# Kernel optimization log

Measured on AMD Instinct MI355X. Metric: run time of the kernel, lower is better.

Reference implementation:

```python
import jax, jax.numpy as jnp
import numpy as np

B, T, D, H = 2, 2048, 1024, 16
HD = D // H  # head dim = 64

def setup_inputs() -> dict:
    key = jax.random.key(0)
    k1, k2, k3 = jax.random.split(key, 3)
    x = jax.random.normal(k1, (B, T, D), dtype=jnp.float32)
    W_qkv = jax.random.normal(k2, (D, 3 * D), dtype=jnp.float32) * 0.02
    b_qkv = jax.random.normal(k3, (3 * D,), dtype=jnp.float32) * 0.02
    return {"x": x, "W_qkv": W_qkv, "b_qkv": b_qkv}

def reference(x, W_qkv, b_qkv):
    Bc, Tc, C = x.shape
    qkv = x @ W_qkv + b_qkv                     # [B,T,3D]
    q, k, v = jnp.split(qkv, 3, axis=-1)        # each [B,T,D]
    def to_heads(t):
        return t.reshape(Bc, Tc, H, HD).transpose(0, 2, 1, 3)  # [B,H,T,hd]
    q, k, v = to_heads(q), to_heads(k), to_heads(v)
    scale = 1.0 / jnp.sqrt(jnp.asarray(HD, dtype=x.dtype))
    att = jnp.einsum('bhqd,bhkd->bhqk', q, k) * scale  # [B,H,T,T]
    att = jax.nn.softmax(att, axis=-1)
    y = jnp.einsum('bhqk,bhkd->bhqd', att, v)          # [B,H,T,hd]
    return y.transpose(0, 2, 1, 3).reshape(Bc, Tc, C)
```

## Files before the change

### kernel.cpp

```cpp
#include <hip/hip_runtime.h>
#include <cstdint>

typedef unsigned short u16;
typedef __bf16 bf16x8 __attribute__((ext_vector_type(8)));
typedef float f32x4 __attribute__((ext_vector_type(4)));
typedef u16 u16x4 __attribute__((ext_vector_type(4)));
typedef u16 u16x8 __attribute__((ext_vector_type(8)));

static __device__ __forceinline__ u16 f2bf(float f) {
  return __builtin_bit_cast(u16, (__bf16)f);
}
static __device__ __forceinline__ float fexp2(float x) {
  float r;
  asm("v_exp_f32 %0, %1" : "=v"(r) : "v"(x));
  return r;
}

#define GLOAD16(gsrc, ldst) \
  __builtin_amdgcn_global_load_lds((const __attribute__((address_space(1))) void*)(gsrc), \
                                   (__attribute__((address_space(3))) void*)(ldst), 16, 0, 0)


__global__ __launch_bounds__(256) void k_prep(const float* __restrict__ x,
                                              const float* __restrict__ W,
                                              u16* __restrict__ xbf,
                                              u16* __restrict__ Wt) {
  __shared__ __align__(16) u16 tile[64 * 72];
  int t = threadIdx.x;
  if (blockIdx.x < 2048) {
    int idx = blockIdx.x * 256 + t;
    const float4* xv = (const float4*)x;
    float4 a = xv[(size_t)idx * 2];
    float4 b = xv[(size_t)idx * 2 + 1];
    u16x8 o;
    o[0]=f2bf(a.x); o[1]=f2bf(a.y); o[2]=f2bf(a.z); o[3]=f2bf(a.w);
    o[4]=f2bf(b.x); o[5]=f2bf(b.y); o[6]=f2bf(b.z); o[7]=f2bf(b.w);
    *(u16x8*)(xbf + (size_t)idx * 8) = o;
    return;
  }
  int bid = blockIdx.x - 2048;
  int bk = bid & 15, bn = bid >> 4;
  int k0 = bk * 64, n0 = bn * 64;
  #pragma unroll
  for (int r = 0; r < 4; r++) {
    int id = r * 256 + t;
    int kl = id >> 4;
    int c  = (id & 15) * 4;
    float4 v = *(const float4*)(W + (size_t)(k0 + kl) * 3072 + n0 + c);
    u16x4 o; o[0]=f2bf(v.x); o[1]=f2bf(v.y); o[2]=f2bf(v.z); o[3]=f2bf(v.w);
    *(u16x4*)(tile + kl * 72 + c) = o;
  }
  __syncthreads();
  #pragma unroll
  for (int r = 0; r < 2; r++) {
    int id = r * 256 + t;
    int nl = id >> 3;
    int w  = id & 7;
    u16x8 o;
    #pragma unroll
    for (int i = 0; i < 8; i++) o[i] = tile[(w * 8 + i) * 72 + nl];
    *(u16x8*)(Wt + (size_t)(n0 + nl) * 1024 + k0 + w * 8) = o;
  }
}

__global__ __launch_bounds__(256) void k_gemm_qkv(const u16* __restrict__ xbf,
                                                  const u16* __restrict__ wt,
                                                  const float* __restrict__ bias,
                                                  u16* __restrict__ qkv,
                                                  u16* __restrict__ vT) {
  __shared__ __align__(16) u16 As[128 * 32];
  __shared__ __align__(16) u16 Bs[128 * 32];
  int bid = blockIdx.x;
  int nt = bid % 24, mt = bid / 24;
  int m0 = mt * 128, n0 = nt * 128;
  int t = threadIdx.x;
  int lane = t & 63, wave = t >> 6;
  int wm = wave >> 1, wn = wave & 1;
  int g = lane >> 4, li = lane & 15;

  f32x4 acc[4][4];
  #pragma unroll
  for (int i = 0; i < 4; i++)
    #pragma unroll
    for (int j = 0; j < 4; j++) acc[i][j] = (f32x4){0.f, 0.f, 0.f, 0.f};

  for (int kt = 0; kt < 32; ++kt) {
    __syncthreads();
    #pragma unroll
    for (int r = 0; r < 2; r++) {
      int p = r * 256 + t;
      int row = p >> 2, w = p & 3;
      int ug = w ^ ((row >> 1) & 3);
      GLOAD16(xbf + (size_t)(m0 + row) * 1024 + kt * 32 + ug * 8, (char*)As + p * 16);
      GLOAD16(wt  + (size_t)(n0 + row) * 1024 + kt * 32 + ug * 8, (char*)Bs + p * 16);
    }
    asm volatile("s_waitcnt vmcnt(0)" ::: "memory");
    __syncthreads();

    bf16x8 af[4], bfr[4];
    #pragma unroll
    for (int mi = 0; mi < 4; mi++) {
      int row = wm * 64 + mi * 16 + li;
      int u = g ^ ((row >> 1) & 3);
      af[mi] = *(const bf16x8*)((const char*)As + row * 64 + u * 16);
    }
    #pragma unroll
    for (int ni = 0; ni < 4; ni++) {
      int row = wn * 64 + ni * 16 + li;
      int u = g ^ ((row >> 1) & 3);
      bfr[ni] = *(const bf16x8*)((const char*)Bs + row * 64 + u * 16);
    }
    #pragma unroll
    for (int mi = 0; mi < 4; mi++)
      #pragma unroll
      for (int ni = 0; ni < 4; ni++)
        acc[mi][ni] = __builtin_amdgcn_mfma_f32_16x16x32_bf16(af[mi], bfr[ni], acc[mi][ni], 0, 0, 0);
  }

  int b = m0 >> 11;
  int tbase = m0 & 2047;
  #pragma unroll
  for (int ni = 0; ni < 4; ni++) {
    int col = n0 + wn * 64 + ni * 16 + li;
    float bv = bias[col];
    float sc = (col < 1024) ? 0.18033688011112042f : 1.0f;
    #pragma unroll
    for (int mi = 0; mi < 4; mi++) {
      int trow = tbase + wm * 64 + mi * 16 + g * 4;
      if (col < 2048) {
        #pragma unroll
        for (int j = 0; j < 4; j++) {
          float v = (acc[mi][ni][j] + bv) * sc;
          qkv[(size_t)(b * 2048 + trow + j) * 3072 + col] = f2bf(v);
        }
      } else {
        u16x4 o;
        #pragma unroll
        for (int j = 0; j < 4; j++) o[j] = f2bf(acc[mi][ni][j] + bv);
        *(u16x4*)(vT + ((size_t)(b * 1024 + (col - 2048))) * 2048 + trow) = o;
      }
    }
  }
}

__global__ __launch_bounds__(256, 2) void k_attn(const u16* __restrict__ qkv,
                                                 const u16* __restrict__ vT,
                                                 float* __restrict__ out) {
  __shared__ __align__(16) u16 smem[32768];
  int bid = blockIdx.x;
  int qt = bid & 15, bh = bid >> 4;
  int b = bh >> 4, h = bh & 15;
  int qbase = qt * 128;
  int t = threadIdx.x, lane = t & 63, wave = t >> 6;
  int g = lane >> 4, li = lane & 15;

  size_t qrowa = (size_t)(b * 2048 + qbase + wave * 32 + li) * 3072 + h * 64;
  bf16x8 qa0 = *(const bf16x8*)(qkv + qrowa + g * 8);
  bf16x8 qa1 = *(const bf16x8*)(qkv + qrowa + 32 + g * 8);
  bf16x8 qb0 = *(const bf16x8*)(qkv + qrowa + 16 * 3072 + g * 8);
  bf16x8 qb1 = *(const bf16x8*)(qkv + qrowa + 16 * 3072 + 32 + g * 8);

  u16x8 ob; 
  #pragma unroll
  for (int i = 0; i < 8; i++) ob[i] = 0x3F80;
  bf16x8 ones = __builtin_bit_cast(bf16x8, ob);

  f32x4 o[2][4];
  #pragma unroll
  for (int f = 0; f < 2; f++)
    #pragma unroll
    for (int i = 0; i < 4; i++) o[f][i] = (f32x4){0.f, 0.f, 0.f, 0.f};
  f32x4 la = (f32x4){0.f, 0.f, 0.f, 0.f}, lb = la;

  const u16* kbase_g = qkv + (size_t)(b * 2048) * 3072 + 1024 + h * 64;
  const u16* vbase_g = vT + (size_t)(bh * 64) * 2048;

  int kRow[4], kUg[4], vRow[4], vUg[4];
  #pragma unroll
  for (int i = 0; i < 4; i++) {
    int p = t + i * 256;
    int kr = p >> 3;
    kRow[i] = (kr & 96) | ((kr & 16) >> 2) | (((kr >> 2) & 3) << 3) | (kr & 3);
    kUg[i] = (p & 7) ^ (kr & 7);
    int vd = p >> 4;
    vRow[i] = vd;
    vUg[i] = (p & 15) ^ (vd & 7);
  }

  auto stage = [&](int key0, int buf) {
    char* kd = (char*)smem + buf * 16384;
    char* vd_ = (char*)smem + 32768 + buf * 16384;
    #pragma unroll
    for (int i = 0; i < 4; i++) {
      int p = t + i * 256;
      GLOAD16(kbase_g + (size_t)(key0 + kRow[i]) * 3072 + kUg[i] * 8, kd + p * 16);
      GLOAD16(vbase_g + (size_t)vRow[i] * 2048 + key0 + vUg[i] * 8, vd_ + p * 16);
    }
  };

  stage(0, 0);
  asm volatile("s_waitcnt vmcnt(0)" ::: "memory");
  __syncthreads();

  #pragma unroll 2
  for (int ph = 0; ph < 16; ++ph) {
    int buf = ph & 1;
    const char* kb = (const char*)smem + buf * 16384;
    const char* vb = (const char*)smem + 32768 + buf * 16384;

    if (ph < 15) stage((ph + 1) * 128, buf ^ 1);

    #pragma unroll
    for (int h2 = 0; h2 < 2; ++h2) {
      const char* kbh = kb + h2 * 8192;
      f32x4 sa[4], sb[4];
      int u0 = g ^ (li & 7);
      __builtin_amdgcn_s_setprio(1);
      #pragma unroll
      for (int st = 0; st < 4; ++st) {
        bf16x8 kf0 = *(const bf16x8*)(kbh + (st * 16 + li) * 128 + u0 * 16);
        bf16x8 kf1 = *(const bf16x8*)(kbh + (st * 16 + li) * 128 + (u0 ^ 4) * 16);
        f32x4 z = (f32x4){0.f, 0.f, 0.f, 0.f};
        sa[st] = __builtin_amdgcn_mfma_f32_16x16x32_bf16(kf0, qa0, z, 0, 0, 0);
        sa[st] = __builtin_amdgcn_mfma_f32_16x16x32_bf16(kf1, qa1, sa[st], 0, 0, 0);
        sb[st] = __builtin_amdgcn_mfma_f32_16x16x32_bf16(kf0, qb0, z, 0, 0, 0);
        sb[st] = __builtin_amdgcn_mfma_f32_16x16x32_bf16(kf1, qb1, sb[st], 0, 0, 0);
      }
      __builtin_amdgcn_s_setprio(0);

      float pa[16], pbf[16];
      #pragma unroll
      for (int i = 0; i < 16; i++) pa[i] = fexp2(sa[i >> 2][i & 3]);
      #pragma unroll
      for (int i = 0; i < 16; i++) pbf[i] = fexp2(sb[i >> 2][i & 3]);

      bf16x8 pba[2], pbb[2];
      #pragma unroll
      for (int c = 0; c < 2; c++)
        #pragma unroll
        for (int e = 0; e < 8; e++) {
          pba[c][e] = (__bf16)pa[c * 8 + e];
          pbb[c][e] = (__bf16)pbf[c * 8 + e];
        }

      __builtin_amdgcn_s_setprio(1);
      la = __builtin_amdgcn_mfma_f32_16x16x32_bf16(ones, pba[0], la, 0, 0, 0);
      la = __builtin_amdgcn_mfma_f32_16x16x32_bf16(ones, pba[1], la, 0, 0, 0);
      lb = __builtin_amdgcn_mfma_f32_16x16x32_bf16(ones, pbb[0], lb, 0, 0, 0);
      lb = __builtin_amdgcn_mfma_f32_16x16x32_bf16(ones, pbb[1], lb, 0, 0, 0);
      #pragma unroll
      for (int c = 0; c < 2; c++) {
        int ucb = h2 * 8 + c * 4 + g;
        #pragma unroll
        for (int dt = 0; dt < 4; dt++) {
          int d = dt * 16 + li;
          bf16x8 vf = *(const bf16x8*)(vb + d * 256 + ((ucb ^ (li & 7)) << 4));
          o[0][dt] = __builtin_amdgcn_mfma_f32_16x16x32_bf16(vf, pba[c], o[0][dt], 0, 0, 0);
          o[1][dt] = __builtin_amdgcn_mfma_f32_16x16x32_bf16(vf, pbb[c], o[1][dt], 0, 0, 0);
        }
      }
      __builtin_amdgcn_s_setprio(0);
    }

    __syncthreads();
  }

  float inva = 1.0f / la[0], invb = 1.0f / lb[0];
  #pragma unroll
  for (int f = 0; f < 2; f++) {
    float inv = f ? invb : inva;
    int ql = wave * 32 + f * 16 + li;
    #pragma unroll
    for (int dt = 0; dt < 4; dt++) {
      int u = dt * 4 + g;
      int up = u ^ (ql & 7);
      f32x4 v = o[f][dt] * inv;
      *(f32x4*)((char*)smem + ql * 256 + up * 16) = v;
    }
  }
  __syncthreads();
  int ql = t >> 1, seg = t & 1;
  size_t obase = (size_t)(b * 2048 + qbase + ql) * 1024 + h * 64;
  #pragma unroll
  for (int i = 0; i < 8; i++) {
    int u = seg * 8 + i;
    int up = u ^ (ql & 7);
    f32x4 v = *(const f32x4*)((const char*)smem + ql * 256 + up * 16);
    *(f32x4*)(out + obase + u * 4) = v;
  }
}

extern "C" void kernel_launch(void* const* d_in, const int* in_sizes, int n_in,
                              void* d_out, int out_size, void* d_ws, size_t ws_size,
                              hipStream_t stream) {
  const float* x    = (const float*)d_in[0];
  const float* W    = (const float*)d_in[1];
  const float* bias = (const float*)d_in[2];
  float* out = (float*)d_out;
  char* ws = (char*)d_ws;
  u16* xbf = (u16*)(ws + 0);
  u16* wt  = (u16*)(ws + 8388608);
  u16* qkv = (u16*)(ws + 14680064);
  u16* vt  = (u16*)(ws + 39845888);

  k_prep<<<2816, 256, 0, stream>>>(x, W, xbf, wt);
  k_gemm_qkv<<<768, 256, 0, stream>>>(xbf, wt, bias, qkv, vt);
  k_attn<<<512, 256, 0, stream>>>(qkv, vt, out);
}
```

Baseline: 93.60 us.

## Retile QKV GEMM to 256x192 with double-buffered LDS and grid swizzle

```diff
diff --git a/kernel.cpp b/kernel.cpp
--- a/kernel.cpp
+++ b/kernel.cpp
@@ -63,70 +63,86 @@
   }
 }
 
-__global__ __launch_bounds__(256) void k_gemm_qkv(const u16* __restrict__ xbf,
-                                                  const u16* __restrict__ wt,
-                                                  const float* __restrict__ bias,
-                                                  u16* __restrict__ qkv,
-                                                  u16* __restrict__ vT) {
-  __shared__ __align__(16) u16 As[128 * 32];
-  __shared__ __align__(16) u16 Bs[128 * 32];
-  int bid = blockIdx.x;
-  int nt = bid % 24, mt = bid / 24;
-  int m0 = mt * 128, n0 = nt * 128;
+__global__ __launch_bounds__(512, 2) void k_gemm_qkv(const u16* __restrict__ xbf,
+                                                     const u16* __restrict__ wt,
+                                                     const float* __restrict__ bias,
+                                                     u16* __restrict__ qkv,
+                                                     u16* __restrict__ vT) {
+  __shared__ __align__(16) u16 As[2 * 256 * 32];
+  __shared__ __align__(16) u16 Bs[2 * 192 * 32];
+  int wg = blockIdx.x;
+  int swz = (wg & 7) * 32 + (wg >> 3);
+  int mt = swz >> 4, nt = swz & 15;
+  int m0 = mt * 256, n0 = nt * 192;
   int t = threadIdx.x;
-  int lane = t & 63, wave = t >> 6;
-  int wm = wave >> 1, wn = wave & 1;
+  int lane = t & 63, wid = t >> 6;
+  int wm = wid >> 2, wn = wid & 3;
   int g = lane >> 4, li = lane & 15;
 
-  f32x4 acc[4][4];
-  #pragma unroll
-  for (int i = 0; i < 4; i++)
-    #pragma unroll
-    for (int j = 0; j < 4; j++) acc[i][j] = (f32x4){0.f, 0.f, 0.f, 0.f};
-
+  f32x4 acc[8][3];
+  #pragma unroll
+  for (int i = 0; i < 8; i++)
+    #pragma unroll
+    for (int j = 0; j < 3; j++) acc[i][j] = (f32x4){0.f, 0.f, 0.f, 0.f};
+
+  auto stage = [&](int kt, int buf) {
+    char* ad = (char*)As + buf * 16384;
+    char* bd = (char*)Bs + buf * 12288;
+    #pragma unroll
+    for (int i = 0; i < 2; i++) {
+      int p = t + i * 512;
+      int row = p >> 2, ug = (p & 3) ^ (row & 3);
+      GLOAD16(xbf + (size_t)(m0 + row) * 1024 + kt * 32 + ug * 8, ad + p * 16);
+    }
+    #pragma unroll
+    for (int i = 0; i < 2; i++) {
+      int p = t + i * 512;
+      if (p < 768) {
+        int row = p >> 2, ug = (p & 3) ^ (row & 3);
+        GLOAD16(wt + (size_t)(n0 + row) * 1024 + kt * 32 + ug * 8, bd + p * 16);
+      }
+    }
+  };
+
+  stage(0, 0);
   for (int kt = 0; kt < 32; ++kt) {
     __syncthreads();
-    #pragma unroll
-    for (int r = 0; r < 2; r++) {
-      int p = r * 256 + t;
-      int row = p >> 2, w = p & 3;
-      int ug = w ^ ((row >> 1) & 3);
-      GLOAD16(xbf + (size_t)(m0 + row) * 1024 + kt * 32 + ug * 8, (char*)As + p * 16);
-      GLOAD16(wt  + (size_t)(n0 + row) * 1024 + kt * 32 + ug * 8, (char*)Bs + p * 16);
-    }
-    asm volatile("s_waitcnt vmcnt(0)" ::: "memory");
-    __syncthreads();
-
-    bf16x8 af[4], bfr[4];
-    #pragma unroll
-    for (int mi = 0; mi < 4; mi++) {
-      int row = wm * 64 + mi * 16 + li;
-      int u = g ^ ((row >> 1) & 3);
-      af[mi] = *(const bf16x8*)((const char*)As + row * 64 + u * 16);
-    }
-    #pragma unroll
-    for (int ni = 0; ni < 4; ni++) {
-      int row = wn * 64 + ni * 16 + li;
-      int u = g ^ ((row >> 1) & 3);
-      bfr[ni] = *(const bf16x8*)((const char*)Bs + row * 64 + u * 16);
-    }
-    #pragma unroll
-    for (int mi = 0; mi < 4; mi++)
-      #pragma unroll
-      for (int ni = 0; ni < 4; ni++)
+    if (kt < 31) stage(kt + 1, (kt & 1) ^ 1);
+    const char* ab = (const char*)As + (kt & 1) * 16384;
+    const char* bb = (const char*)Bs + (kt & 1) * 12288;
+
+    bf16x8 af[8], bfr[3];
+    #pragma unroll
+    for (int mi = 0; mi < 8; mi++) {
+      int row = wm * 128 + mi * 16 + li;
+      int u = g ^ (row & 3);
+      af[mi] = *(const bf16x8*)(ab + row * 64 + u * 16);
+    }
+    #pragma unroll
+    for (int ni = 0; ni < 3; ni++) {
+      int row = wn * 48 + ni * 16 + li;
+      int u = g ^ (row & 3);
+      bfr[ni] = *(const bf16x8*)(bb + row * 64 + u * 16);
+    }
+    __builtin_amdgcn_s_setprio(1);
+    #pragma unroll
+    for (int mi = 0; mi < 8; mi++)
+      #pragma unroll
+      for (int ni = 0; ni < 3; ni++)
         acc[mi][ni] = __builtin_amdgcn_mfma_f32_16x16x32_bf16(af[mi], bfr[ni], acc[mi][ni], 0, 0, 0);
+    __builtin_amdgcn_s_setprio(0);
   }
 
   int b = m0 >> 11;
   int tbase = m0 & 2047;
   #pragma unroll
-  for (int ni = 0; ni < 4; ni++) {
-    int col = n0 + wn * 64 + ni * 16 + li;
+  for (int ni = 0; ni < 3; ni++) {
+    int col = n0 + wn * 48 + ni * 16 + li;
     float bv = bias[col];
     float sc = (col < 1024) ? 0.18033688011112042f : 1.0f;
     #pragma unroll
-    for (int mi = 0; mi < 4; mi++) {
-      int trow = tbase + wm * 64 + mi * 16 + g * 4;
+    for (int mi = 0; mi < 8; mi++) {
+      int trow = tbase + wm * 128 + mi * 16 + g * 4;
       if (col < 2048) {
         #pragma unroll
         for (int j = 0; j < 4; j++) {
@@ -160,7 +176,7 @@
   bf16x8 qb0 = *(const bf16x8*)(qkv + qrowa + 16 * 3072 + g * 8);
   bf16x8 qb1 = *(const bf16x8*)(qkv + qrowa + 16 * 3072 + 32 + g * 8);
 
-  u16x8 ob; 
+  u16x8 ob;
   #pragma unroll
   for (int i = 0; i < 8; i++) ob[i] = 0x3F80;
   bf16x8 ones = __builtin_bit_cast(bf16x8, ob);
@@ -210,29 +226,32 @@
 
     if (ph < 15) stage((ph + 1) * 128, buf ^ 1);
 
+    f32x4 sa[2][4], sb[2][4];
+    int u0 = g ^ (li & 7);
+    __builtin_amdgcn_s_setprio(1);
     #pragma unroll
     for (int h2 = 0; h2 < 2; ++h2) {
       const char* kbh = kb + h2 * 8192;
-      f32x4 sa[4], sb[4];
-      int u0 = g ^ (li & 7);
-      __builtin_amdgcn_s_setprio(1);
       #pragma unroll
       for (int st = 0; st < 4; ++st) {
         bf16x8 kf0 = *(const bf16x8*)(kbh + (st * 16 + li) * 128 + u0 * 16);
         bf16x8 kf1 = *(const bf16x8*)(kbh + (st * 16 + li) * 128 + (u0 ^ 4) * 16);
         f32x4 z = (f32x4){0.f, 0.f, 0.f, 0.f};
-        sa[st] = __builtin_amdgcn_mfma_f32_16x16x32_bf16(kf0, qa0, z, 0, 0, 0);
-        sa[st] = __builtin_amdgcn_mfma_f32_16x16x32_bf16(kf1, qa1, sa[st], 0, 0, 0);
-        sb[st] = __builtin_amdgcn_mfma_f32_16x16x32_bf16(kf0, qb0, z, 0, 0, 0);
-        sb[st] = __builtin_amdgcn_mfma_f32_16x16x32_bf16(kf1, qb1, sb[st], 0, 0, 0);
+        sa[h2][st] = __builtin_amdgcn_mfma_f32_16x16x32_bf16(kf0, qa0, z, 0, 0, 0);
+        sa[h2][st] = __builtin_amdgcn_mfma_f32_16x16x32_bf16(kf1, qa1, sa[h2][st], 0, 0, 0);
+        sb[h2][st] = __builtin_amdgcn_mfma_f32_16x16x32_bf16(kf0, qb0, z, 0, 0, 0);
+        sb[h2][st] = __builtin_amdgcn_mfma_f32_16x16x32_bf16(kf1, qb1, sb[h2][st], 0, 0, 0);
       }
-      __builtin_amdgcn_s_setprio(0);
-
+    }
+    __builtin_amdgcn_s_setprio(0);
+
+    #pragma unroll
+    for (int h2 = 0; h2 < 2; ++h2) {
       float pa[16], pbf[16];
       #pragma unroll
-      for (int i = 0; i < 16; i++) pa[i] = fexp2(sa[i >> 2][i & 3]);
-      #pragma unroll
-      for (int i = 0; i < 16; i++) pbf[i] = fexp2(sb[i >> 2][i & 3]);
+      for (int i = 0; i < 16; i++) pa[i] = fexp2(sa[h2][i >> 2][i & 3]);
+      #pragma unroll
+      for (int i = 0; i < 16; i++) pbf[i] = fexp2(sb[h2][i >> 2][i & 3]);
 
       bf16x8 pba[2], pbb[2];
       #pragma unroll
@@ -304,6 +323,6 @@
   u16* vt  = (u16*)(ws + 39845888);
 
   k_prep<<<2816, 256, 0, stream>>>(x, W, xbf, wt);
-  k_gemm_qkv<<<768, 256, 0, stream>>>(xbf, wt, bias, qkv, vt);
+  k_gemm_qkv<<<256, 512, 0, stream>>>(xbf, wt, bias, qkv, vt);
   k_attn<<<512, 256, 0, stream>>>(qkv, vt, out);
 }
```

New measurement: 101.3 us. 8.3% more time.
